# Performance work log

Hardware: AMD Instinct MI355X
Metric: run time of the kernel (lower is better)

Reference implementation:

```python
import jax, jax.numpy as jnp
import numpy as np

D_MODEL = 1024
N_HEADS = 16
D_K = D_MODEL // N_HEADS
D_FF = 4096
B, S = 2, 2048
LN_EPS = 1e-5
NEG_INF = -1e30  # finite stand-in for -inf; first (all-masked) row is overwritten by zeros anyway


def layer_norm(x, g, b):
    mu = jnp.mean(x, axis=-1, keepdims=True)
    var = jnp.mean(jnp.square(x - mu), axis=-1, keepdims=True)
    return (x - mu) * jax.lax.rsqrt(var + LN_EPS) * g + b


def setup_inputs() -> dict:
    key = jax.random.key(0)
    ks = jax.random.split(key, 16)
    sd = 0.02
    inp = {
        "query": jax.random.normal(ks[0], (B, S, D_MODEL), jnp.float32),
        "key": jax.random.normal(ks[1], (B, S, D_MODEL), jnp.float32),
        "values": jax.random.normal(ks[2], (B, S, D_MODEL), jnp.float32),
        "Wq": jax.random.normal(ks[3], (D_MODEL, D_MODEL), jnp.float32) * sd,
        "bq": jnp.zeros((D_MODEL,), jnp.float32),
        "Wk": jax.random.normal(ks[4], (D_MODEL, D_MODEL), jnp.float32) * sd,
        "bk": jnp.zeros((D_MODEL,), jnp.float32),
        "Wv": jax.random.normal(ks[5], (D_MODEL, D_MODEL), jnp.float32) * sd,
        "bv": jnp.zeros((D_MODEL,), jnp.float32),
        "Wo": jax.random.normal(ks[6], (D_MODEL, D_MODEL), jnp.float32) * sd,
        "bo": jnp.zeros((D_MODEL,), jnp.float32),
        "ln1_g": jnp.ones((D_MODEL,), jnp.float32),
        "ln1_b": jnp.zeros((D_MODEL,), jnp.float32),
        "W1": jax.random.normal(ks[7], (D_MODEL, D_FF), jnp.float32) * sd,
        "b1": jnp.zeros((D_FF,), jnp.float32),
        "W2": jax.random.normal(ks[8], (D_FF, D_MODEL), jnp.float32) * sd,
        "b2": jnp.zeros((D_MODEL,), jnp.float32),
        "ln2_g": jnp.ones((D_MODEL,), jnp.float32),
        "ln2_b": jnp.zeros((D_MODEL,), jnp.float32),
        "mask": 0,
    }
    return inp


def reference(query, key, values, Wq, bq, Wk, bk, Wv, bv, Wo, bo,
              ln1_g, ln1_b, W1, b1, W2, b2, ln2_g, ln2_b, mask):
    b, s, d = query.shape
    # projections -> [B, H, S, d_k]
    q = (query @ Wq + bq).reshape(b, s, N_HEADS, D_K).transpose(0, 2, 1, 3)
    k = (key @ Wk + bk).reshape(b, s, N_HEADS, D_K).transpose(0, 2, 1, 3)
    v = (values @ Wv + bv).reshape(b, s, N_HEADS, D_K).transpose(0, 2, 1, 3)
    # scores [B, H, S, S]
    scores = jnp.einsum("bhqd,bhkd->bhqk", q, k) / jnp.sqrt(jnp.float32(D_K))
    # torch: triu(ones, k=mask)==0 -> allowed iff j < i + mask
    i = jnp.arange(s)[:, None]
    j = jnp.arange(s)[None, :]
    allowed = j < (i + mask)
    scores = jnp.where(allowed, scores, NEG_INF)
    attn = jax.nn.softmax(scores, axis=-1)
    if mask == 0:
        # zero-pad trick: first query row (fully masked) is replaced by zeros
        attn = attn.at[:, :, 0, :].set(0.0)
    ctx = jnp.einsum("bhqk,bhkd->bhqd", attn, v)
    ctx = ctx.transpose(0, 2, 1, 3).reshape(b, s, d)
    attn_out = ctx @ Wo + bo
    x = layer_norm(query + attn_out, ln1_g, ln1_b)
    ffn = jax.nn.relu(x @ W1 + b1) @ W2 + b2
    out = layer_norm(x + ffn, ln2_g, ln2_b)
    return out
```

## Files before the change

### kernel.cpp

```cpp
#include <hip/hip_runtime.h>


typedef __attribute__((ext_vector_type(8))) __bf16 bf16x8;
typedef __attribute__((ext_vector_type(4))) float f32x4;
typedef __attribute__((ext_vector_type(8))) short s16x8;

struct alignas(8)  S4 { short x, y, z, w; };
struct alignas(16) F4 { float x, y, z, w; };

static __device__ __forceinline__ short f2bf(float f) {
  unsigned u = __float_as_uint(f);
  u += 0x7fff + ((u >> 16) & 1);
  return (short)(u >> 16);
}

static __device__ __forceinline__ short f2bf_fast(float f) {
  union { __bf16 h; short s; } u;
  u.h = (__bf16)f;
  return u.s;
}

#if __has_builtin(__builtin_amdgcn_exp2f)
#define EXP2F(x) __builtin_amdgcn_exp2f(x)
#else
#define EXP2F(x) exp2f(x)
#endif
#define SM_SCALE 0.18033688011112042f

static __device__ __forceinline__ void store_out(float* p, float v) { *p = v; }
static __device__ __forceinline__ void store_out(short* p, float v) { *p = f2bf(v); }

#define GLL16(g, l)                                                         \
  __builtin_amdgcn_global_load_lds(                                         \
      (__attribute__((address_space(1))) void*)(g),                         \
      (__attribute__((address_space(3))) void*)(l), 16, 0, 0)

__global__ __launch_bounds__(256) void cvt_bf16_kernel(
    const float* __restrict__ i0, const float* __restrict__ i1,
    const float* __restrict__ i2, short* __restrict__ o0,
    short* __restrict__ o1, short* __restrict__ o2) {
  int z = blockIdx.y;
  const float* in = z == 0 ? i0 : (z == 1 ? i1 : i2);
  short* out = z == 0 ? o0 : (z == 1 ? o1 : o2);
  int i = (blockIdx.x * 256 + threadIdx.x) * 4;
  F4 v = *(const F4*)(in + i);
  S4 o = { f2bf(v.x), f2bf(v.y), f2bf(v.z), f2bf(v.w) };
  *(S4*)(out + i) = o;
}

__global__ __launch_bounds__(256) void transpose_cvt_kernel(
    const float* __restrict__ Wq, const float* __restrict__ Wk,
    const float* __restrict__ Wv, const float* __restrict__ Wo,
    const float* __restrict__ W1, const float* __restrict__ W2,
    short* __restrict__ Wqt, short* __restrict__ Wkt,
    short* __restrict__ Wvt, short* __restrict__ Wot,
    short* __restrict__ W1t, short* __restrict__ W2t) {
  __shared__ float tile[64][65];
  int bid = blockIdx.x;
  const float* W; short* Wt; int K, N, kx, ny;
  if (bid < 1024) {
    int w = bid >> 8, t = bid & 255;
    W = w == 0 ? Wq : (w == 1 ? Wk : (w == 2 ? Wv : Wo));
    Wt = w == 0 ? Wqt : (w == 1 ? Wkt : (w == 2 ? Wvt : Wot));
    K = 1024; N = 1024; kx = t & 15; ny = t >> 4;
  } else if (bid < 2048) {
    int t = bid - 1024;
    W = W1; Wt = W1t; K = 1024; N = 4096; kx = t & 15; ny = t >> 4;
  } else {
    int t = bid - 2048;
    W = W2; Wt = W2t; K = 4096; N = 1024; kx = t & 63; ny = t >> 6;
  }
  int k0 = kx * 64, n0 = ny * 64;
  int tid = threadIdx.x;
  int rr = tid >> 4, cc = (tid & 15) * 4;
#pragma unroll
  for (int p = 0; p < 4; ++p) {
    int row = p * 16 + rr;
    F4 v = *(const F4*)&W[(long)(k0 + row) * N + n0 + cc];
    tile[row][cc] = v.x; tile[row][cc + 1] = v.y;
    tile[row][cc + 2] = v.z; tile[row][cc + 3] = v.w;
  }
  __syncthreads();
#pragma unroll
  for (int p = 0; p < 4; ++p) {
    int rn = p * 16 + rr;
    S4 o = { f2bf(tile[cc + 0][rn]), f2bf(tile[cc + 1][rn]),
             f2bf(tile[cc + 2][rn]), f2bf(tile[cc + 3][rn]) };
    *(S4*)&Wt[(long)(n0 + rn) * K + k0 + cc] = o;
  }
}

template <int OUT_MODE, bool RELU, typename OT>
__device__ __forceinline__ void gemm256c_core(
    const short* __restrict__ A, const short* __restrict__ Bt,
    const float* __restrict__ bias, OT* __restrict__ out,
    int N, int K, int kBeg, int kEnd, int m0, int n0) {
  __shared__ __align__(16) short sA[2][256 * 64];
  __shared__ __align__(16) short sB[2][256 * 64];
  int tid = threadIdx.x;
  int lane = tid & 63, wave = tid >> 6;
  int col = lane & 15, quad = lane >> 4;
  int wm = (wave >> 2) * 128;
  int wn = (wave & 3) * 64;

  f32x4 acc[8][4] = {};
  const int NT = (kEnd - kBeg) >> 6;
  const int t0 = kBeg >> 6;

  auto stageA = [&](int buf, int kt) {
#pragma unroll
    for (int j = 0; j < 4; ++j) {
      int idx = j * 512 + tid;
      int row = idx >> 3, cp = idx & 7;
      int c = cp ^ (row & 7);
      GLL16(A + (long)(m0 + row) * K + kt * 64 + c * 8,
            &sA[buf][(j * 512 + (wave << 6)) * 8]);
    }
  };
  auto stageB = [&](int buf, int kt) {
#pragma unroll
    for (int j = 0; j < 4; ++j) {
      int idx = j * 512 + tid;
      int row = idx >> 3, cp = idx & 7;
      int c = cp ^ (row & 7);
      GLL16(Bt + (long)(n0 + row) * K + kt * 64 + c * 8,
            &sB[buf][(j * 512 + (wave << 6)) * 8]);
    }
  };

  stageA(0, t0);     stageB(0, t0);
  stageA(1, t0 + 1); stageB(1, t0 + 1);
  asm volatile("s_waitcnt vmcnt(8)" ::: "memory");
  __builtin_amdgcn_s_barrier();

  for (int t = 0; t < NT; ++t) {
    int cur = t & 1;
    bool pf = (t + 2 < NT);
    bf16x8 bf[4][2], af[8][2];

#pragma unroll
    for (int n = 0; n < 4; ++n) {
      int rb = wn + n * 16 + col;
#pragma unroll
      for (int kk = 0; kk < 2; ++kk) {
        int ca = kk * 4 + quad;
        bf[n][kk] = *(const bf16x8*)&sB[cur][rb * 64 + ((ca ^ (rb & 7)) << 3)];
      }
    }
#pragma unroll
    for (int m = 0; m < 8; ++m) {
      int ra = wm + m * 16 + col;
#pragma unroll
      for (int kk = 0; kk < 2; ++kk) {
        int ca = kk * 4 + quad;
        af[m][kk] = *(const bf16x8*)&sA[cur][ra * 64 + ((ca ^ (ra & 7)) << 3)];
      }
    }
    asm volatile("s_waitcnt lgkmcnt(0)" ::: "memory");
    __builtin_amdgcn_s_barrier();
    __builtin_amdgcn_sched_barrier(0);
    if (pf) { stageA(cur, t0 + t + 2); stageB(cur, t0 + t + 2); }
    __builtin_amdgcn_s_setprio(1);
#pragma unroll
    for (int m = 0; m < 8; ++m)
#pragma unroll
      for (int n = 0; n < 4; ++n)
#pragma unroll
        for (int kk = 0; kk < 2; ++kk)
          acc[m][n] = __builtin_amdgcn_mfma_f32_16x16x32_bf16(
              af[m][kk], bf[n][kk], acc[m][n], 0, 0, 0);
    __builtin_amdgcn_s_setprio(0);
    if (pf) asm volatile("s_waitcnt vmcnt(8)" ::: "memory");
    else    asm volatile("s_waitcnt vmcnt(0)" ::: "memory");
    __builtin_amdgcn_s_barrier();
  }

#pragma unroll
  for (int m = 0; m < 8; ++m) {
#pragma unroll
    for (int n = 0; n < 4; ++n) {
      int Cc = n0 + wn + n * 16 + col;
      float bv = bias ? bias[Cc] : 0.f;
#pragma unroll
      for (int r = 0; r < 4; ++r) {
        int R = m0 + wm + m * 16 + quad * 4 + r;
        float v = acc[m][n][r] + bv;
        if (RELU) v = v > 0.f ? v : 0.f;
        if (OUT_MODE == 0) {
          store_out(&out[(long)R * N + Cc], v);
        } else {
          int bb = R >> 11, s = R & 2047, h = Cc >> 6, d = Cc & 63;
          store_out(&out[((long)((bb * 16 + h) * 2048 + s) << 6) + d], v);
        }
      }
    }
  }
}

__device__ __forceinline__ void gsp128_core(
    const short* __restrict__ A, const short* __restrict__ Bt,
    const float* __restrict__ bias, float* __restrict__ out,
    int N, int K, int kBeg, int kEnd, int m0, int n0) {
  __shared__ __align__(16) short sA[2][256 * 64];
  __shared__ __align__(16) short sB[2][128 * 64];
  int tid = threadIdx.x;
  int lane = tid & 63, wave = tid >> 6;
  int col = lane & 15, quad = lane >> 4;
  int wm = (wave >> 1) * 64;
  int wn = (wave & 1) * 64;

  f32x4 acc[4][4] = {};
  const int NT = (kEnd - kBeg) >> 6;
  const int t0 = kBeg >> 6;

  auto stageA = [&](int buf, int kt) {
#pragma unroll
    for (int j = 0; j < 4; ++j) {
      int idx = j * 512 + tid;
      int row = idx >> 3, cp = idx & 7;
      int c = cp ^ (row & 7);
      GLL16(A + (long)(m0 + row) * K + kt * 64 + c * 8,
            &sA[buf][(j * 512 + (wave << 6)) * 8]);
    }
  };
  auto stageB = [&](int buf, int kt) {
#pragma unroll
    for (int j = 0; j < 2; ++j) {
      int idx = j * 512 + tid;
      int row = idx >> 3, cp = idx & 7;
      int c = cp ^ (row & 7);
      GLL16(Bt + (long)(n0 + row) * K + kt * 64 + c * 8,
            &sB[buf][(j * 512 + (wave << 6)) * 8]);
    }
  };

  stageA(0, t0);     stageB(0, t0);
  stageA(1, t0 + 1); stageB(1, t0 + 1);
  asm volatile("s_waitcnt vmcnt(6)" ::: "memory");
  __builtin_amdgcn_s_barrier();

  for (int t = 0; t < NT; ++t) {
    int cur = t & 1;
    bool pf = (t + 2 < NT);
    bf16x8 bf[4][2], af[4][2];

#pragma unroll
    for (int n = 0; n < 4; ++n) {
      int rb = wn + n * 16 + col;
#pragma unroll
      for (int kk = 0; kk < 2; ++kk) {
        int ca = kk * 4 + quad;
        bf[n][kk] = *(const bf16x8*)&sB[cur][rb * 64 + ((ca ^ (rb & 7)) << 3)];
      }
    }
#pragma unroll
    for (int m = 0; m < 4; ++m) {
      int ra = wm + m * 16 + col;
#pragma unroll
      for (int kk = 0; kk < 2; ++kk) {
        int ca = kk * 4 + quad;
        af[m][kk] = *(const bf16x8*)&sA[cur][ra * 64 + ((ca ^ (ra & 7)) << 3)];
      }
    }
    asm volatile("s_waitcnt lgkmcnt(0)" ::: "memory");
    __builtin_amdgcn_s_barrier();
    __builtin_amdgcn_sched_barrier(0);
    if (pf) { stageA(cur, t0 + t + 2); stageB(cur, t0 + t + 2); }
    __builtin_amdgcn_s_setprio(1);
#pragma unroll
    for (int m = 0; m < 4; ++m)
#pragma unroll
      for (int n = 0; n < 4; ++n)
#pragma unroll
        for (int kk = 0; kk < 2; ++kk)
          acc[m][n] = __builtin_amdgcn_mfma_f32_16x16x32_bf16(
              af[m][kk], bf[n][kk], acc[m][n], 0, 0, 0);
    __builtin_amdgcn_s_setprio(0);
    if (pf) asm volatile("s_waitcnt vmcnt(6)" ::: "memory");
    else    asm volatile("s_waitcnt vmcnt(0)" ::: "memory");
    __builtin_amdgcn_s_barrier();
  }

#pragma unroll
  for (int m = 0; m < 4; ++m) {
#pragma unroll
    for (int n = 0; n < 4; ++n) {
      int Cc = n0 + wn + n * 16 + col;
      float bv = bias ? bias[Cc] : 0.f;
#pragma unroll
      for (int r = 0; r < 4; ++r) {
        int R = m0 + wm + m * 16 + quad * 4 + r;
        out[(long)R * N + Cc] = acc[m][n][r] + bv;
      }
    }
  }
}

__global__ __launch_bounds__(512) void g256c_ffn1(
    const short* __restrict__ A, const short* __restrict__ Bt,
    const float* __restrict__ bias, short* __restrict__ out) {
  gemm256c_core<0, true, short>(A, Bt, bias, out, 4096, 1024, 0, 1024,
                                blockIdx.x * 256, blockIdx.y * 256);
}

__global__ __launch_bounds__(512) void g256c_qkv(
    const short* __restrict__ Aq, const short* __restrict__ Ak,
    const short* __restrict__ Av, const short* __restrict__ Btq,
    const short* __restrict__ Btk, const short* __restrict__ Btv,
    const float* __restrict__ bq, const float* __restrict__ bk,
    const float* __restrict__ bv, short* __restrict__ Qp,
    short* __restrict__ Kp, short* __restrict__ Vp) {
  int z = blockIdx.z;
  const short* A = z == 0 ? Aq : (z == 1 ? Ak : Av);
  const short* Bt = z == 0 ? Btq : (z == 1 ? Btk : Btv);
  const float* bias = z == 0 ? bq : (z == 1 ? bk : bv);
  short* out = z == 0 ? Qp : (z == 1 ? Kp : Vp);
  gemm256c_core<1, false, short>(A, Bt, bias, out, 1024, 1024, 0, 1024,
                                 blockIdx.x * 256, blockIdx.y * 256);
}

__global__ __launch_bounds__(512) void gsp_wo(
    const short* __restrict__ A, const short* __restrict__ Bt,
    const float* __restrict__ bias, float* __restrict__ p0,
    float* __restrict__ p1) {
  int z = blockIdx.z;
  float* out = z == 0 ? p0 : p1;
  const float* b = z == 0 ? bias : nullptr;
  gsp128_core(A, Bt, b, out, 1024, 1024, z * 512, z * 512 + 512,
              blockIdx.x * 256, blockIdx.y * 128);
}

__global__ __launch_bounds__(512) void gsp_ffn2(
    const short* __restrict__ A, const short* __restrict__ Bt,
    const float* __restrict__ bias, float* __restrict__ p0,
    float* __restrict__ p1) {
  int z = blockIdx.z;
  float* out = z == 0 ? p0 : p1;
  const float* b = z == 0 ? bias : nullptr;
  gsp128_core(A, Bt, b, out, 1024, 4096, z * 2048, z * 2048 + 2048,
              blockIdx.x * 256, blockIdx.y * 128);
}

__global__ __launch_bounds__(256) void attn_kernel(
    const short* __restrict__ Q, const short* __restrict__ K,
    const short* __restrict__ V, const int* __restrict__ maskp,
    short* __restrict__ ctx) {
  __shared__ __align__(16) short sK[2][64 * 64];
  __shared__ __align__(16) int   sVt[2][64 * 32];
  __shared__ __align__(16) short sP[4 * 32 * 64];
  __shared__ float sLred[64];
  int tid = threadIdx.x, wave = tid >> 6;
  int lane = tid & 63;
  int col = lane & 15, quad = lane >> 4;
  int wlow = wave >> 1, g = wave & 1;
  int bh = blockIdx.x, pair = blockIdx.y;
  int maskv = maskp[0];
  const long base = (long)bh * (2048 * 64);
  int b = bh >> 4, h = bh & 15;

  int kp = tid & 31, dg = tid >> 5, d0v = dg * 8;

  for (int pass = 0; pass < 2; ++pass) {
    int qt = pass ? (31 - pair) : pair;
    int iq0 = qt * 64 + wlow * 32;

    long jmax = (long)qt * 64 + 63 + maskv - 1;
    int tot = (jmax < 0) ? 0 : (int)(jmax >> 6) + 1;
    if (tot > 32) tot = 32;

    bf16x8 aQ[2][2];
#pragma unroll
    for (int mt = 0; mt < 2; ++mt)
#pragma unroll
      for (int kk = 0; kk < 2; ++kk)
        aQ[mt][kk] = *(const bf16x8*)&Q[base +
            (long)(iq0 + mt * 16 + col) * 64 + kk * 32 + quad * 8];

    f32x4 o[2][4] = {};
    float lsum[2][4] = {};

    if (tot > 0) {
#pragma unroll
      for (int j = 0; j < 2; ++j) {
        int idx = j * 256 + tid;
        int row = idx >> 3, cp = idx & 7;
        int c = cp ^ (row & 7);
        GLL16(K + base + (long)row * 64 + c * 8,
              &sK[0][(j * 256 + (wave << 6)) * 8]);
      }
      {
        s16x8 u0 = *(const s16x8*)&V[base + (long)(2 * kp) * 64 + d0v];
        s16x8 u1 = *(const s16x8*)&V[base + (long)(2 * kp + 1) * 64 + d0v];
#pragma unroll
        for (int j = 0; j < 8; ++j) {
          int d = d0v + j;
          int w = ((int)(unsigned short)u1[j] << 16) | (unsigned short)u0[j];
          sVt[0][d * 32 + ((((kp >> 2) ^ (d & 7)) << 2) | (kp & 3))] = w;
        }
      }
    }
    __syncthreads();

    for (int kt = 0; kt < tot; ++kt) {
      int cur = kt & 1, nxt = cur ^ 1;
      bool pf = (kt + 1 < tot);

      s16x8 u0, u1;
      if (pf) {
#pragma unroll
        for (int j = 0; j < 2; ++j) {
          int idx = j * 256 + tid;
          int row = idx >> 3, cp = idx & 7;
          int c = cp ^ (row & 7);
          GLL16(K + base + (long)((kt + 1) * 64 + row) * 64 + c * 8,
                &sK[nxt][(j * 256 + (wave << 6)) * 8]);
        }
        u0 = *(const s16x8*)&V[base + (long)((kt + 1) * 64 + 2 * kp) * 64 + d0v];
        u1 = *(const s16x8*)&V[base + (long)((kt + 1) * 64 + 2 * kp + 1) * 64 + d0v];
      }

      f32x4 sc[2][2] = {};
      __builtin_amdgcn_s_setprio(1);
#pragma unroll
      for (int kk = 0; kk < 2; ++kk) {
        int ca = kk * 4 + quad;
#pragma unroll
        for (int nt = 0; nt < 2; ++nt) {
          int rk = (2 * g + nt) * 16 + col;
          bf16x8 bK = *(const bf16x8*)&sK[cur][rk * 64 + ((ca ^ (rk & 7)) << 3)];
#pragma unroll
          for (int mt = 0; mt < 2; ++mt)
            sc[mt][nt] = __builtin_amdgcn_mfma_f32_16x16x32_bf16(
                aQ[mt][kk], bK, sc[mt][nt], 0, 0, 0);
        }
      }
      __builtin_amdgcn_s_setprio(0);

      bool interior = (kt * 64 + g * 32 + 31) < (iq0 + maskv);
      if (interior) {
#pragma unroll
        for (int mt = 0; mt < 2; ++mt)
#pragma unroll
          for (int r = 0; r < 4; ++r) {
            int qr = mt * 16 + quad * 4 + r;
#pragma unroll
            for (int nt = 0; nt < 2; ++nt) {
              float p = EXP2F(sc[mt][nt][r] * SM_SCALE);
              lsum[mt][r] += p;
              int k8 = 4 * g + nt * 2 + (col >> 3);
              sP[wave * 2048 + qr * 64 + (((k8 ^ (qr & 7)) << 3) | (col & 7))] =
                  f2bf_fast(p);
            }
          }
      } else {
#pragma unroll
        for (int mt = 0; mt < 2; ++mt)
#pragma unroll
          for (int r = 0; r < 4; ++r) {
            int i = iq0 + mt * 16 + quad * 4 + r;
            int qr = mt * 16 + quad * 4 + r;
#pragma unroll
            for (int nt = 0; nt < 2; ++nt) {
              int j = kt * 64 + (2 * g + nt) * 16 + col;
              float p = (j < i + maskv) ? EXP2F(sc[mt][nt][r] * SM_SCALE) : 0.f;
              lsum[mt][r] += p;
              int k8 = 4 * g + nt * 2 + (col >> 3);
              sP[wave * 2048 + qr * 64 + (((k8 ^ (qr & 7)) << 3) | (col & 7))] =
                  f2bf_fast(p);
            }
          }
      }

      {
        int ca = 4 * g + quad;
        bf16x8 bV[4];
#pragma unroll
        for (int dt = 0; dt < 4; ++dt) {
          int d = dt * 16 + col;
          bV[dt] = *(const bf16x8*)((const short*)sVt[cur] + d * 64 +
                                    ((ca ^ (d & 7)) << 3));
        }
        __builtin_amdgcn_s_setprio(1);
#pragma unroll
        for (int mt = 0; mt < 2; ++mt) {
          int rp = mt * 16 + col;
          bf16x8 aP = *(const bf16x8*)&sP[wave * 2048 + rp * 64 +
                                          ((ca ^ (rp & 7)) << 3)];
#pragma unroll
          for (int dt = 0; dt < 4; ++dt)
            o[mt][dt] = __builtin_amdgcn_mfma_f32_16x16x32_bf16(
                aP, bV[dt], o[mt][dt], 0, 0, 0);
        }
        __builtin_amdgcn_s_setprio(0);
      }

      if (pf) {
#pragma unroll
        for (int j = 0; j < 8; ++j) {
          int d = d0v + j;
          int w = ((int)(unsigned short)u1[j] << 16) | (unsigned short)u0[j];
          sVt[nxt][d * 32 + ((((kp >> 2) ^ (d & 7)) << 2) | (kp & 3))] = w;
        }
      }
      __syncthreads();
    }

#pragma unroll
    for (int mt = 0; mt < 2; ++mt)
#pragma unroll
      for (int r = 0; r < 4; ++r)
#pragma unroll
        for (int off = 1; off < 16; off <<= 1)
          lsum[mt][r] += __shfl_xor(lsum[mt][r], off);

    f32x4* odv = (f32x4*)sP;
    int slot = wlow * 64 + lane;
    if (g == 1) {
#pragma unroll
      for (int mt = 0; mt < 2; ++mt)
#pragma unroll
        for (int dt = 0; dt < 4; ++dt)
          odv[(mt * 4 + dt) * 128 + slot] = o[mt][dt];
      if (col == 0) {
#pragma unroll
        for (int mt = 0; mt < 2; ++mt)
#pragma unroll
          for (int r = 0; r < 4; ++r)
            sLred[wlow * 32 + mt * 16 + quad * 4 + r] = lsum[mt][r];
      }
    }
    __syncthreads();
    if (g == 0) {
#pragma unroll
      for (int mt = 0; mt < 2; ++mt)
#pragma unroll
        for (int dt = 0; dt < 4; ++dt)
          o[mt][dt] += odv[(mt * 4 + dt) * 128 + slot];
#pragma unroll
      for (int mt = 0; mt < 2; ++mt)
#pragma unroll
        for (int r = 0; r < 4; ++r) {
          float ls = lsum[mt][r] + sLred[wlow * 32 + mt * 16 + quad * 4 + r];
          int i = iq0 + mt * 16 + quad * 4 + r;
          float inv = (ls > 0.f) ? 1.f / ls : 0.f;
          if (maskv == 0 && i == 0) inv = 0.f;
#pragma unroll
          for (int dt = 0; dt < 4; ++dt)
            ctx[(long)(b * 2048 + i) * 1024 + h * 64 + dt * 16 + col] =
                f2bf(o[mt][dt][r] * inv);
        }
    }
    __syncthreads();
  }
}

__global__ __launch_bounds__(256) void ln_comb_kernel(
    const float* __restrict__ p0, const float* __restrict__ p1,
    const float* __restrict__ res, const float* __restrict__ g,
    const float* __restrict__ b, float* __restrict__ outf,
    short* __restrict__ outb) {
  int r = blockIdx.x, tid = threadIdx.x;
  int lane = tid & 63, wave = tid >> 6;
  long off0 = (long)r * 1024;
  F4 a = ((const F4*)(p0 + off0))[tid];
  F4 c = ((const F4*)(p1 + off0))[tid];
  F4 d = ((const F4*)(res + off0))[tid];
  F4 v = { a.x + c.x + d.x, a.y + c.y + d.y, a.z + c.z + d.z, a.w + c.w + d.w };
  float s = v.x + v.y + v.z + v.w;
  float sq = v.x * v.x + v.y * v.y + v.z * v.z + v.w * v.w;
#pragma unroll
  for (int off = 1; off < 64; off <<= 1) {
    s += __shfl_xor(s, off);
    sq += __shfl_xor(sq, off);
  }
  __shared__ float rs[4], rq[4];
  if (lane == 0) { rs[wave] = s; rq[wave] = sq; }
  __syncthreads();
  s = rs[0] + rs[1] + rs[2] + rs[3];
  sq = rq[0] + rq[1] + rq[2] + rq[3];
  float mu = s * (1.0f / 1024.0f);
  float var = sq * (1.0f / 1024.0f) - mu * mu;
  float rstd = rsqrtf(var + 1e-5f);
  F4 gv = ((const F4*)g)[tid], bv = ((const F4*)b)[tid];
  F4 o;
  o.x = (v.x - mu) * rstd * gv.x + bv.x;
  o.y = (v.y - mu) * rstd * gv.y + bv.y;
  o.z = (v.z - mu) * rstd * gv.z + bv.z;
  o.w = (v.w - mu) * rstd * gv.w + bv.w;
  ((F4*)(outf + off0))[tid] = o;
  if (outb) {
    S4 ob = { f2bf(o.x), f2bf(o.y), f2bf(o.z), f2bf(o.w) };
    ((S4*)(outb + off0))[tid] = ob;
  }
}

extern "C" void kernel_launch(void* const* d_in, const int* in_sizes, int n_in,
                              void* d_out, int out_size, void* d_ws, size_t ws_size,
                              hipStream_t stream) {
  const float* query  = (const float*)d_in[0];
  const float* keyi   = (const float*)d_in[1];
  const float* values = (const float*)d_in[2];
  const float* Wq = (const float*)d_in[3];
  const float* bq = (const float*)d_in[4];
  const float* Wk = (const float*)d_in[5];
  const float* bk = (const float*)d_in[6];
  const float* Wv = (const float*)d_in[7];
  const float* bv = (const float*)d_in[8];
  const float* Wo = (const float*)d_in[9];
  const float* bo = (const float*)d_in[10];
  const float* ln1_g = (const float*)d_in[11];
  const float* ln1_b = (const float*)d_in[12];
  const float* W1 = (const float*)d_in[13];
  const float* b1 = (const float*)d_in[14];
  const float* W2 = (const float*)d_in[15];
  const float* b2 = (const float*)d_in[16];
  const float* ln2_g = (const float*)d_in[17];
  const float* ln2_b = (const float*)d_in[18];
  const int*   maskp = (const int*)d_in[19];
  float* out = (float*)d_out;

  char* ws = (char*)d_ws;
  const size_t MB = 1u << 20;
  short* q_bf = (short*)(ws + 0);
  short* k_bf = (short*)(ws + 8 * MB);
  short* v_bf = (short*)(ws + 16 * MB);
  short* ctx  = (short*)(ws + 24 * MB);
  short* Qp   = (short*)(ws + 32 * MB);
  short* Kp   = (short*)(ws + 40 * MB);
  short* Vp   = (short*)(ws + 48 * MB);
  short* Wqt  = (short*)(ws + 56 * MB);
  short* Wkt  = (short*)(ws + 58 * MB);
  short* Wvt  = (short*)(ws + 60 * MB);
  short* Wot  = (short*)(ws + 62 * MB);
  short* W1t  = (short*)(ws + 64 * MB);
  short* W2t  = (short*)(ws + 72 * MB);
  short* hbuf = (short*)(ws + 80 * MB);
  float* pWo0 = (float*)(ws + 0);
  float* pWo1 = (float*)(ws + 32 * MB);
  float* x_f32 = (float*)(ws + 16 * MB);
  short* x_bf  = (short*)(ws + 48 * MB);
  float* pF0 = (float*)(ws + 0);
  float* pF1 = (float*)(ws + 32 * MB);

  cvt_bf16_kernel<<<dim3(4096, 3), 256, 0, stream>>>(query, keyi, values,
                                                     q_bf, k_bf, v_bf);
  transpose_cvt_kernel<<<3072, 256, 0, stream>>>(Wq, Wk, Wv, Wo, W1, W2,
                                                 Wqt, Wkt, Wvt, Wot, W1t, W2t);
  g256c_qkv<<<dim3(16, 4, 3), 512, 0, stream>>>(q_bf, k_bf, v_bf,
                                                Wqt, Wkt, Wvt,
                                                bq, bk, bv, Qp, Kp, Vp);
  attn_kernel<<<dim3(32, 16), 256, 0, stream>>>(Qp, Kp, Vp, maskp, ctx);
  gsp_wo<<<dim3(16, 8, 2), 512, 0, stream>>>(ctx, Wot, bo, pWo0, pWo1);
  ln_comb_kernel<<<4096, 256, 0, stream>>>(pWo0, pWo1, query, ln1_g, ln1_b,
                                           x_f32, x_bf);
  g256c_ffn1<<<dim3(16, 16), 512, 0, stream>>>(x_bf, W1t, b1, hbuf);
  gsp_ffn2<<<dim3(16, 8, 2), 512, 0, stream>>>(hbuf, W2t, b2, pF0, pF1);
  ln_comb_kernel<<<4096, 256, 0, stream>>>(pF0, pF1, x_f32, ln2_g, ln2_b,
                                           out, nullptr);

  (void)in_sizes; (void)n_in; (void)out_size; (void)ws_size;
}
```

Baseline: 370.4 us.

## Replace 256-tile GEMMs with unified 128x128 4-wave GEMM and merge prep kernels

All four GEMMs (QKV, Wo, FFN1, FFN2) now use a single 128x128-tile, 256-thread core instead of 256x256 and 256x128 tiles with 512 threads. This gives each launch many more blocks and uses less LDS per block, so more blocks fit per CU and the many CUs are better filled. The cost is lower data reuse per tile and more global and L2 traffic. The input conversion and weight transpose kernels are also merged into one launch to save one launch.

Result: faster. 362.8 us (-2.0%).

```diff
diff --git a/kernel.cpp b/kernel.cpp
--- a/kernel.cpp
+++ b/kernel.cpp
@@ -35,20 +35,10 @@
       (__attribute__((address_space(1))) void*)(g),                         \
       (__attribute__((address_space(3))) void*)(l), 16, 0, 0)
 
-__global__ __launch_bounds__(256) void cvt_bf16_kernel(
+__global__ __launch_bounds__(256) void prep_kernel(
     const float* __restrict__ i0, const float* __restrict__ i1,
     const float* __restrict__ i2, short* __restrict__ o0,
-    short* __restrict__ o1, short* __restrict__ o2) {
-  int z = blockIdx.y;
-  const float* in = z == 0 ? i0 : (z == 1 ? i1 : i2);
-  short* out = z == 0 ? o0 : (z == 1 ? o1 : o2);
-  int i = (blockIdx.x * 256 + threadIdx.x) * 4;
-  F4 v = *(const F4*)(in + i);
-  S4 o = { f2bf(v.x), f2bf(v.y), f2bf(v.z), f2bf(v.w) };
-  *(S4*)(out + i) = o;
-}
-
-__global__ __launch_bounds__(256) void transpose_cvt_kernel(
+    short* __restrict__ o1, short* __restrict__ o2,
     const float* __restrict__ Wq, const float* __restrict__ Wk,
     const float* __restrict__ Wv, const float* __restrict__ Wo,
     const float* __restrict__ W1, const float* __restrict__ W2,
@@ -56,7 +46,19 @@
     short* __restrict__ Wvt, short* __restrict__ Wot,
     short* __restrict__ W1t, short* __restrict__ W2t) {
   __shared__ float tile[64][65];
-  int bid = blockIdx.x;
+  int bid0 = blockIdx.x;
+  int tid = threadIdx.x;
+  if (bid0 < 12288) {
+    int z = bid0 >> 12, x = bid0 & 4095;
+    const float* in = z == 0 ? i0 : (z == 1 ? i1 : i2);
+    short* out = z == 0 ? o0 : (z == 1 ? o1 : o2);
+    int i = (x * 256 + tid) * 4;
+    F4 v = *(const F4*)(in + i);
+    S4 o = { f2bf(v.x), f2bf(v.y), f2bf(v.z), f2bf(v.w) };
+    *(S4*)(out + i) = o;
+    return;
+  }
+  int bid = bid0 - 12288;
   const float* W; short* Wt; int K, N, kx, ny;
   if (bid < 1024) {
     int w = bid >> 8, t = bid & 255;
@@ -71,7 +73,6 @@
     W = W2; Wt = W2t; K = 4096; N = 1024; kx = t & 63; ny = t >> 6;
   }
   int k0 = kx * 64, n0 = ny * 64;
-  int tid = threadIdx.x;
   int rr = tid >> 4, cc = (tid & 15) * 4;
 #pragma unroll
   for (int p = 0; p < 4; ++p) {
@@ -91,40 +92,40 @@
 }
 
 template <int OUT_MODE, bool RELU, typename OT>
-__device__ __forceinline__ void gemm256c_core(
+__device__ __forceinline__ void gsp128b_core(
     const short* __restrict__ A, const short* __restrict__ Bt,
     const float* __restrict__ bias, OT* __restrict__ out,
     int N, int K, int kBeg, int kEnd, int m0, int n0) {
-  __shared__ __align__(16) short sA[2][256 * 64];
-  __shared__ __align__(16) short sB[2][256 * 64];
+  __shared__ __align__(16) short sA[2][128 * 64];
+  __shared__ __align__(16) short sB[2][128 * 64];
   int tid = threadIdx.x;
   int lane = tid & 63, wave = tid >> 6;
   int col = lane & 15, quad = lane >> 4;
-  int wm = (wave >> 2) * 128;
-  int wn = (wave & 3) * 64;
-
-  f32x4 acc[8][4] = {};
+  int wm = (wave >> 1) * 64;
+  int wn = (wave & 1) * 64;
+
+  f32x4 acc[4][4] = {};
   const int NT = (kEnd - kBeg) >> 6;
   const int t0 = kBeg >> 6;
 
   auto stageA = [&](int buf, int kt) {
 #pragma unroll
     for (int j = 0; j < 4; ++j) {
-      int idx = j * 512 + tid;
+      int idx = j * 256 + tid;
       int row = idx >> 3, cp = idx & 7;
       int c = cp ^ (row & 7);
       GLL16(A + (long)(m0 + row) * K + kt * 64 + c * 8,
-            &sA[buf][(j * 512 + (wave << 6)) * 8]);
+            &sA[buf][(j * 256 + (wave << 6)) * 8]);
     }
   };
   auto stageB = [&](int buf, int kt) {
 #pragma unroll
     for (int j = 0; j < 4; ++j) {
-      int idx = j * 512 + tid;
+      int idx = j * 256 + tid;
       int row = idx >> 3, cp = idx & 7;
       int c = cp ^ (row & 7);
       GLL16(Bt + (long)(n0 + row) * K + kt * 64 + c * 8,
-            &sB[buf][(j * 512 + (wave << 6)) * 8]);
+            &sB[buf][(j * 256 + (wave << 6)) * 8]);
     }
   };
 
@@ -136,7 +137,7 @@
   for (int t = 0; t < NT; ++t) {
     int cur = t & 1;
     bool pf = (t + 2 < NT);
-    bf16x8 bf[4][2], af[8][2];
+    bf16x8 bf[4][2], af[4][2];
 
 #pragma unroll
     for (int n = 0; n < 4; ++n) {
@@ -148,8 +149,8 @@
       }
     }
 #pragma unroll
-    for (int m = 0; m < 8; ++m) {
-      int ra = wm + m * 16 + col;
+    for (int m = 0; m < 4; ++m) {
+      int ra = wm + (m & 1) * 16 + (m >> 1) * 32 + col;
 #pragma unroll
       for (int kk = 0; kk < 2; ++kk) {
         int ca = kk * 4 + quad;
@@ -162,7 +163,7 @@
     if (pf) { stageA(cur, t0 + t + 2); stageB(cur, t0 + t + 2); }
     __builtin_amdgcn_s_setprio(1);
 #pragma unroll
-    for (int m = 0; m < 8; ++m)
+    for (int m = 0; m < 4; ++m)
 #pragma unroll
       for (int n = 0; n < 4; ++n)
 #pragma unroll
@@ -176,14 +177,15 @@
   }
 
 #pragma unroll
-  for (int m = 0; m < 8; ++m) {
+  for (int m = 0; m < 4; ++m) {
+    int rbase = wm + (m & 1) * 16 + (m >> 1) * 32;
 #pragma unroll
     for (int n = 0; n < 4; ++n) {
       int Cc = n0 + wn + n * 16 + col;
       float bv = bias ? bias[Cc] : 0.f;
 #pragma unroll
       for (int r = 0; r < 4; ++r) {
-        int R = m0 + wm + m * 16 + quad * 4 + r;
+        int R = m0 + rbase + quad * 4 + r;
         float v = acc[m][n][r] + bv;
         if (RELU) v = v > 0.f ? v : 0.f;
         if (OUT_MODE == 0) {
@@ -197,113 +199,7 @@
   }
 }
 
-__device__ __forceinline__ void gsp128_core(
-    const short* __restrict__ A, const short* __restrict__ Bt,
-    const float* __restrict__ bias, float* __restrict__ out,
-    int N, int K, int kBeg, int kEnd, int m0, int n0) {
-  __shared__ __align__(16) short sA[2][256 * 64];
-  __shared__ __align__(16) short sB[2][128 * 64];
-  int tid = threadIdx.x;
-  int lane = tid & 63, wave = tid >> 6;
-  int col = lane & 15, quad = lane >> 4;
-  int wm = (wave >> 1) * 64;
-  int wn = (wave & 1) * 64;
-
-  f32x4 acc[4][4] = {};
-  const int NT = (kEnd - kBeg) >> 6;
-  const int t0 = kBeg >> 6;
-
-  auto stageA = [&](int buf, int kt) {
-#pragma unroll
-    for (int j = 0; j < 4; ++j) {
-      int idx = j * 512 + tid;
-      int row = idx >> 3, cp = idx & 7;
-      int c = cp ^ (row & 7);
-      GLL16(A + (long)(m0 + row) * K + kt * 64 + c * 8,
-            &sA[buf][(j * 512 + (wave << 6)) * 8]);
-    }
-  };
-  auto stageB = [&](int buf, int kt) {
-#pragma unroll
-    for (int j = 0; j < 2; ++j) {
-      int idx = j * 512 + tid;
-      int row = idx >> 3, cp = idx & 7;
-      int c = cp ^ (row & 7);
-      GLL16(Bt + (long)(n0 + row) * K + kt * 64 + c * 8,
-            &sB[buf][(j * 512 + (wave << 6)) * 8]);
-    }
-  };
-
-  stageA(0, t0);     stageB(0, t0);
-  stageA(1, t0 + 1); stageB(1, t0 + 1);
-  asm volatile("s_waitcnt vmcnt(6)" ::: "memory");
-  __builtin_amdgcn_s_barrier();
-
-  for (int t = 0; t < NT; ++t) {
-    int cur = t & 1;
-    bool pf = (t + 2 < NT);
-    bf16x8 bf[4][2], af[4][2];
-
-#pragma unroll
-    for (int n = 0; n < 4; ++n) {
-      int rb = wn + n * 16 + col;
-#pragma unroll
-      for (int kk = 0; kk < 2; ++kk) {
-        int ca = kk * 4 + quad;
-        bf[n][kk] = *(const bf16x8*)&sB[cur][rb * 64 + ((ca ^ (rb & 7)) << 3)];
-      }
-    }
-#pragma unroll
-    for (int m = 0; m < 4; ++m) {
-      int ra = wm + m * 16 + col;
-#pragma unroll
-      for (int kk = 0; kk < 2; ++kk) {
-        int ca = kk * 4 + quad;
-        af[m][kk] = *(const bf16x8*)&sA[cur][ra * 64 + ((ca ^ (ra & 7)) << 3)];
-      }
-    }
-    asm volatile("s_waitcnt lgkmcnt(0)" ::: "memory");
-    __builtin_amdgcn_s_barrier();
-    __builtin_amdgcn_sched_barrier(0);
-    if (pf) { stageA(cur, t0 + t + 2); stageB(cur, t0 + t + 2); }
-    __builtin_amdgcn_s_setprio(1);
-#pragma unroll
-    for (int m = 0; m < 4; ++m)
-#pragma unroll
-      for (int n = 0; n < 4; ++n)
-#pragma unroll
-        for (int kk = 0; kk < 2; ++kk)
-          acc[m][n] = __builtin_amdgcn_mfma_f32_16x16x32_bf16(
-              af[m][kk], bf[n][kk], acc[m][n], 0, 0, 0);
-    __builtin_amdgcn_s_setprio(0);
-    if (pf) asm volatile("s_waitcnt vmcnt(6)" ::: "memory");
-    else    asm volatile("s_waitcnt vmcnt(0)" ::: "memory");
-    __builtin_amdgcn_s_barrier();
-  }
-
-#pragma unroll
-  for (int m = 0; m < 4; ++m) {
-#pragma unroll
-    for (int n = 0; n < 4; ++n) {
-      int Cc = n0 + wn + n * 16 + col;
-      float bv = bias ? bias[Cc] : 0.f;
-#pragma unroll
-      for (int r = 0; r < 4; ++r) {
-        int R = m0 + wm + m * 16 + quad * 4 + r;
-        out[(long)R * N + Cc] = acc[m][n][r] + bv;
-      }
-    }
-  }
-}
-
-__global__ __launch_bounds__(512) void g256c_ffn1(
-    const short* __restrict__ A, const short* __restrict__ Bt,
-    const float* __restrict__ bias, short* __restrict__ out) {
-  gemm256c_core<0, true, short>(A, Bt, bias, out, 4096, 1024, 0, 1024,
-                                blockIdx.x * 256, blockIdx.y * 256);
-}
-
-__global__ __launch_bounds__(512) void g256c_qkv(
+__global__ __launch_bounds__(256) void gsp_qkv(
     const short* __restrict__ Aq, const short* __restrict__ Ak,
     const short* __restrict__ Av, const short* __restrict__ Btq,
     const short* __restrict__ Btk, const short* __restrict__ Btv,
@@ -315,30 +211,39 @@
   const short* Bt = z == 0 ? Btq : (z == 1 ? Btk : Btv);
   const float* bias = z == 0 ? bq : (z == 1 ? bk : bv);
   short* out = z == 0 ? Qp : (z == 1 ? Kp : Vp);
-  gemm256c_core<1, false, short>(A, Bt, bias, out, 1024, 1024, 0, 1024,
-                                 blockIdx.x * 256, blockIdx.y * 256);
-}
-
-__global__ __launch_bounds__(512) void gsp_wo(
+  gsp128b_core<1, false, short>(A, Bt, bias, out, 1024, 1024, 0, 1024,
+                                blockIdx.x * 128, blockIdx.y * 128);
+}
+
+__global__ __launch_bounds__(256) void gsp_wo(
     const short* __restrict__ A, const short* __restrict__ Bt,
     const float* __restrict__ bias, float* __restrict__ p0,
     float* __restrict__ p1) {
   int z = blockIdx.z;
   float* out = z == 0 ? p0 : p1;
   const float* b = z == 0 ? bias : nullptr;
-  gsp128_core(A, Bt, b, out, 1024, 1024, z * 512, z * 512 + 512,
-              blockIdx.x * 256, blockIdx.y * 128);
-}
-
-__global__ __launch_bounds__(512) void gsp_ffn2(
+  gsp128b_core<0, false, float>(A, Bt, b, out, 1024, 1024,
+                                z * 512, z * 512 + 512,
+                                blockIdx.x * 128, blockIdx.y * 128);
+}
+
+__global__ __launch_bounds__(256) void gsp_ffn1(
+    const short* __restrict__ A, const short* __restrict__ Bt,
+    const float* __restrict__ bias, short* __restrict__ out) {
+  gsp128b_core<0, true, short>(A, Bt, bias, out, 4096, 1024, 0, 1024,
+                               blockIdx.x * 128, blockIdx.y * 128);
+}
+
+__global__ __launch_bounds__(256) void gsp_ffn2(
     const short* __restrict__ A, const short* __restrict__ Bt,
     const float* __restrict__ bias, float* __restrict__ p0,
     float* __restrict__ p1) {
   int z = blockIdx.z;
   float* out = z == 0 ? p0 : p1;
   const float* b = z == 0 ? bias : nullptr;
-  gsp128_core(A, Bt, b, out, 1024, 4096, z * 2048, z * 2048 + 2048,
-              blockIdx.x * 256, blockIdx.y * 128);
+  gsp128b_core<0, false, float>(A, Bt, b, out, 1024, 4096,
+                                z * 2048, z * 2048 + 2048,
+                                blockIdx.x * 128, blockIdx.y * 128);
 }
 
 __global__ __launch_bounds__(256) void attn_kernel(
@@ -642,19 +547,19 @@
   float* pF0 = (float*)(ws + 0);
   float* pF1 = (float*)(ws + 32 * MB);
 
-  cvt_bf16_kernel<<<dim3(4096, 3), 256, 0, stream>>>(query, keyi, values,
-                                                     q_bf, k_bf, v_bf);
-  transpose_cvt_kernel<<<3072, 256, 0, stream>>>(Wq, Wk, Wv, Wo, W1, W2,
-                                                 Wqt, Wkt, Wvt, Wot, W1t, W2t);
-  g256c_qkv<<<dim3(16, 4, 3), 512, 0, stream>>>(q_bf, k_bf, v_bf,
-                                                Wqt, Wkt, Wvt,
-                                                bq, bk, bv, Qp, Kp, Vp);
+  prep_kernel<<<15360, 256, 0, stream>>>(query, keyi, values,
+                                         q_bf, k_bf, v_bf,
+                                         Wq, Wk, Wv, Wo, W1, W2,
+                                         Wqt, Wkt, Wvt, Wot, W1t, W2t);
+  gsp_qkv<<<dim3(32, 8, 3), 256, 0, stream>>>(q_bf, k_bf, v_bf,
+                                              Wqt, Wkt, Wvt,
+                                              bq, bk, bv, Qp, Kp, Vp);
   attn_kernel<<<dim3(32, 16), 256, 0, stream>>>(Qp, Kp, Vp, maskp, ctx);
-  gsp_wo<<<dim3(16, 8, 2), 512, 0, stream>>>(ctx, Wot, bo, pWo0, pWo1);
+  gsp_wo<<<dim3(32, 8, 2), 256, 0, stream>>>(ctx, Wot, bo, pWo0, pWo1);
   ln_comb_kernel<<<4096, 256, 0, stream>>>(pWo0, pWo1, query, ln1_g, ln1_b,
                                            x_f32, x_bf);
-  g256c_ffn1<<<dim3(16, 16), 512, 0, stream>>>(x_bf, W1t, b1, hbuf);
-  gsp_ffn2<<<dim3(16, 8, 2), 512, 0, stream>>>(hbuf, W2t, b2, pF0, pF1);
+  gsp_ffn1<<<dim3(32, 32), 256, 0, stream>>>(x_bf, W1t, b1, hbuf);
+  gsp_ffn2<<<dim3(32, 8, 2), 256, 0, stream>>>(hbuf, W2t, b2, pF0, pF1);
   ln_comb_kernel<<<4096, 256, 0, stream>>>(pF0, pF1, x_f32, ln2_g, ln2_b,
                                            out, nullptr);
 
```
